# Optimization experiments

Hardware: AMD Instinct MI355X
Metric: run time of the kernel (lower is better)

Reference implementation:

```python
import jax, jax.numpy as jnp
import numpy as np

B, D = 65536, 1024
E, U, T = 10, 10, 2  # experts, expert units, tasks


def setup_inputs() -> dict:
    key = jax.random.key(0)
    ks = jax.random.split(key, 8)
    s = 0.02
    return {
        "x": jax.random.normal(ks[0], (B, D), dtype=jnp.float32),
        "show_index": jax.random.randint(ks[1], (B,), 0, 100),
        "st": jax.random.normal(ks[2], (B, 16), dtype=jnp.float32),
        "expert_w": jax.random.normal(ks[3], (E, D, U), dtype=jnp.float32) * s,
        "expert_b": jnp.zeros((E, U), dtype=jnp.float32),
        "gate_w": jax.random.normal(ks[4], (T, D, E), dtype=jnp.float32) * s,
        "gate_b": jnp.zeros((T, E), dtype=jnp.float32),
        "ctr_w": jax.random.normal(ks[5], (U, 1), dtype=jnp.float32) * s,
        "ctr_b": jnp.zeros((1,), dtype=jnp.float32),
        "cvr_w": jax.random.normal(ks[6], (U, 1), dtype=jnp.float32) * s,
        "cvr_b": jnp.zeros((1,), dtype=jnp.float32),
    }


def reference(x, show_index, st, expert_w, expert_b, gate_w, gate_b,
              ctr_w, ctr_b, cvr_w, cvr_b):
    # experts_output[b, u, e] = relu(x @ W_e + b_e)  (stacked on axis 2)
    experts_output = jax.nn.relu(
        jnp.einsum("bd,edu->bue", x, expert_w) + expert_b.T[None, :, :]
    )  # [B, U, E]
    # gates[b, t, e] = softmax over experts
    gates = jax.nn.softmax(
        jnp.einsum("bd,tde->bte", x, gate_w) + gate_b[None, :, :], axis=-1
    )  # [B, T, E]
    # weighted sum over experts for each task: [B, T, U]
    task_inputs = jnp.einsum("bue,bte->btu", experts_output, gates)
    ctr_logits = jax.nn.sigmoid(task_inputs[:, 0, :] @ ctr_w + ctr_b)  # [B, 1]
    cvr_logits = jax.nn.sigmoid(task_inputs[:, 1, :] @ cvr_w + cvr_b)  # [B, 1]
    return (ctr_logits, cvr_logits)
```

## Files before the change

kernel.cpp:

```cpp
#include <hip/hip_runtime.h>
#include <hip/hip_bf16.h>

#define B_ROWS 65536
#define D_DIM  1024
#define NC     120
#define NCP    128
#define MBLK   64
#define BK     64
#define ASTR   72
#define CSTR   121

typedef __attribute__((ext_vector_type(4))) float f32x4;
typedef __attribute__((ext_vector_type(8))) short bf16x8;

__device__ __forceinline__ unsigned short f2bf(float f) {
  union { float f; unsigned u; } v; v.f = f;
  unsigned r = v.u + 0x7FFFu + ((v.u >> 16) & 1u);
  return (unsigned short)(r >> 16);
}

__global__ __launch_bounds__(256) void pack_w(const float* __restrict__ ew,
                                              const float* __restrict__ gw,
                                              short* __restrict__ wt) {
  int idx = blockIdx.x * 256 + threadIdx.x;
  int c = idx >> 10, d = idx & 1023;
  float v = 0.f;
  if (c < 100) {
    int e = c / 10, u = c % 10;
    v = ew[(e * D_DIM + d) * 10 + u];
  } else if (c < NC) {
    int q = c - 100; int t = q / 10, e = q % 10;
    v = gw[(t * D_DIM + d) * 10 + e];
  }
  wt[c * D_DIM + d] = (short)f2bf(v);
}

union Smem {
  struct { short A[MBLK * ASTR]; short Bm[NCP * ASTR]; } s;
  float C[MBLK * CSTR];
};

__global__ __launch_bounds__(256) void mmoe_main(
    const float* __restrict__ x, const short* __restrict__ wt,
    const float* __restrict__ eb, const float* __restrict__ gb,
    const float* __restrict__ ctr_w, const float* __restrict__ ctr_b,
    const float* __restrict__ cvr_w, const float* __restrict__ cvr_b,
    float* __restrict__ out) {
  __shared__ Smem sm;
  const int tid  = threadIdx.x;
  const int wave = tid >> 6, lane = tid & 63;
  const int m0   = blockIdx.x * MBLK;

  const int arow = tid >> 4;
  const int akp  = (tid & 15) * 4;
  const int bc   = tid >> 3;
  const int bks  = (tid & 7) * 8;

  const int lhi = lane >> 4;
  const int llo = lane & 15;

  f32x4 acc[8];
  const f32x4 vzero = {0.f, 0.f, 0.f, 0.f};
  #pragma unroll
  for (int i = 0; i < 8; ++i) acc[i] = vzero;

  for (int k0 = 0; k0 < D_DIM; k0 += BK) {
    __syncthreads();
    #pragma unroll
    for (int j = 0; j < 4; ++j) {
      const int row = j * 16 + arow;
      const float4 v = *reinterpret_cast<const float4*>(
          x + (size_t)(m0 + row) * D_DIM + k0 + akp);
      ushort4 h;
      h.x = f2bf(v.x); h.y = f2bf(v.y); h.z = f2bf(v.z); h.w = f2bf(v.w);
      *reinterpret_cast<ushort4*>(&sm.s.A[row * ASTR + akp]) = h;
    }
    #pragma unroll
    for (int j = 0; j < 4; ++j) {
      const int c = j * 32 + bc;
      const uint4 v = *reinterpret_cast<const uint4*>(wt + c * D_DIM + k0 + bks);
      *reinterpret_cast<uint4*>(&sm.s.Bm[c * ASTR + bks]) = v;
    }
    __syncthreads();
    #pragma unroll
    for (int ks = 0; ks < BK; ks += 32) {
      const bf16x8 af = *reinterpret_cast<const bf16x8*>(
          &sm.s.A[(wave * 16 + llo) * ASTR + ks + lhi * 8]);
      #pragma unroll
      for (int ct = 0; ct < 8; ++ct) {
        const bf16x8 bf = *reinterpret_cast<const bf16x8*>(
            &sm.s.Bm[(ct * 16 + llo) * ASTR + ks + lhi * 8]);
        acc[ct] = __builtin_amdgcn_mfma_f32_16x16x32_bf16(af, bf, acc[ct], 0, 0, 0);
      }
    }
  }

  __syncthreads();
  #pragma unroll
  for (int ct = 0; ct < 8; ++ct) {
    const int col = ct * 16 + llo;
    if (col < NC) {
      #pragma unroll
      for (int r = 0; r < 4; ++r) {
        const int row = wave * 16 + lhi * 4 + r;
        sm.C[row * CSTR + col] = acc[ct][r];
      }
    }
  }
  __syncthreads();

  if (tid < MBLK) {
    const float* crow = &sm.C[tid * CSTR];
    float w0[10], w1[10];
    #pragma unroll
    for (int u = 0; u < 10; ++u) { w0[u] = ctr_w[u]; w1[u] = cvr_w[u]; }
    float s0[10], s1[10];
    #pragma unroll
    for (int e = 0; e < 10; ++e) {
      float a0 = 0.f, a1 = 0.f;
      #pragma unroll
      for (int u = 0; u < 10; ++u) {
        float v = crow[e * 10 + u] + eb[e * 10 + u];
        v = fmaxf(v, 0.f);
        a0 = fmaf(v, w0[u], a0);
        a1 = fmaf(v, w1[u], a1);
      }
      s0[e] = a0; s1[e] = a1;
    }
    {
      float gl[10], mx = -1e30f;
      #pragma unroll
      for (int e = 0; e < 10; ++e) { gl[e] = crow[100 + e] + gb[e]; mx = fmaxf(mx, gl[e]); }
      float den = 0.f, num = 0.f;
      #pragma unroll
      for (int e = 0; e < 10; ++e) {
        float p = __expf(gl[e] - mx); den += p; num = fmaf(p, s0[e], num);
      }
      float z = num / den + ctr_b[0];
      out[m0 + tid] = 1.f / (1.f + __expf(-z));
    }
    {
      float gl[10], mx = -1e30f;
      #pragma unroll
      for (int e = 0; e < 10; ++e) { gl[e] = crow[110 + e] + gb[10 + e]; mx = fmaxf(mx, gl[e]); }
      float den = 0.f, num = 0.f;
      #pragma unroll
      for (int e = 0; e < 10; ++e) {
        float p = __expf(gl[e] - mx); den += p; num = fmaf(p, s1[e], num);
      }
      float z = num / den + cvr_b[0];
      out[B_ROWS + m0 + tid] = 1.f / (1.f + __expf(-z));
    }
  }
}

extern "C" void kernel_launch(void* const* d_in, const int* in_sizes, int n_in,
                              void* d_out, int out_size, void* d_ws, size_t ws_size,
                              hipStream_t stream) {
  const float* x     = (const float*)d_in[0];
  const float* ew    = (const float*)d_in[3];
  const float* eb    = (const float*)d_in[4];
  const float* gw    = (const float*)d_in[5];
  const float* gb    = (const float*)d_in[6];
  const float* ctr_w = (const float*)d_in[7];
  const float* ctr_b = (const float*)d_in[8];
  const float* cvr_w = (const float*)d_in[9];
  const float* cvr_b = (const float*)d_in[10];
  float* out = (float*)d_out;
  short* wt  = (short*)d_ws;

  pack_w<<<512, 256, 0, stream>>>(ew, gw, wt);
  mmoe_main<<<B_ROWS / MBLK, 256, 0, stream>>>(x, wt, eb, gb, ctr_w, ctr_b,
                                               cvr_w, cvr_b, out);
}
```

Measured before the change: 398.1 us.

## Double-buffer weight tiles via direct global-to-LDS loads and register A operands

Replaces the single-buffered LDS staging of both x and weights with a two-stage pipeline. Weight tiles are copied straight into LDS with global_load_lds into an XOR-swizzled layout, prepared by the pack kernel, to avoid bank conflicts without padding. x is read directly into registers in MFMA operand order and converted to bf16 there, skipping the LDS round trip. The epilogue now splits the two tasks across 128 threads, and an occupancy hint of 4 blocks per CU is added, which costs more registers for the prefetched A fragments.

```diff
diff --git a/kernel.cpp b/kernel.cpp
--- a/kernel.cpp
+++ b/kernel.cpp
@@ -1,13 +1,10 @@
 #include <hip/hip_runtime.h>
-#include <hip/hip_bf16.h>
 
 #define B_ROWS 65536
 #define D_DIM  1024
 #define NC     120
-#define NCP    128
 #define MBLK   64
 #define BK     64
-#define ASTR   72
 #define CSTR   121
 
 typedef __attribute__((ext_vector_type(4))) float f32x4;
@@ -17,6 +14,15 @@
   union { float f; unsigned u; } v; v.f = f;
   unsigned r = v.u + 0x7FFFu + ((v.u >> 16) & 1u);
   return (unsigned short)(r >> 16);
+}
+
+__device__ __forceinline__ bf16x8 cvt8(float4 p, float4 q) {
+  bf16x8 r;
+  r[0] = (short)f2bf(p.x); r[1] = (short)f2bf(p.y);
+  r[2] = (short)f2bf(p.z); r[3] = (short)f2bf(p.w);
+  r[4] = (short)f2bf(q.x); r[5] = (short)f2bf(q.y);
+  r[6] = (short)f2bf(q.z); r[7] = (short)f2bf(q.w);
+  return r;
 }
 
 __global__ __launch_bounds__(256) void pack_w(const float* __restrict__ ew,
@@ -32,15 +38,22 @@
     int q = c - 100; int t = q / 10, e = q % 10;
     v = gw[(t * D_DIM + d) * 10 + e];
   }
-  wt[c * D_DIM + d] = (short)f2bf(v);
+  wt[c * D_DIM + (d ^ ((c & 7) << 3))] = (short)f2bf(v);
 }
 
-union Smem {
-  struct { short A[MBLK * ASTR]; short Bm[NCP * ASTR]; } s;
+union __align__(16) Smem {
+  struct { short B0[128 * 64]; short B1[128 * 64]; } s;
   float C[MBLK * CSTR];
 };
 
-__global__ __launch_bounds__(256) void mmoe_main(
+typedef const __attribute__((address_space(1))) void as1_cvoid;
+typedef __attribute__((address_space(3))) void as3_void;
+
+__device__ __forceinline__ void gload_lds16(const void* g, void* l) {
+  __builtin_amdgcn_global_load_lds((as1_cvoid*)g, (as3_void*)l, 16, 0, 0);
+}
+
+__global__ __launch_bounds__(256, 4) void mmoe_main(
     const float* __restrict__ x, const short* __restrict__ wt,
     const float* __restrict__ eb, const float* __restrict__ gb,
     const float* __restrict__ ctr_w, const float* __restrict__ ctr_b,
@@ -49,108 +62,115 @@
   __shared__ Smem sm;
   const int tid  = threadIdx.x;
   const int wave = tid >> 6, lane = tid & 63;
+  const int lhi  = lane >> 4, llo = lane & 15;
   const int m0   = blockIdx.x * MBLK;
+  const int bswz = (llo & 7) << 3;
 
-  const int arow = tid >> 4;
-  const int akp  = (tid & 15) * 4;
-  const int bc   = tid >> 3;
-  const int bks  = (tid & 7) * 8;
+  const float* ax = x + (size_t)(m0 + wave * 16 + llo) * D_DIM + lhi * 8;
 
-  const int lhi = lane >> 4;
-  const int llo = lane & 15;
+  const short* bsrc = wt + (lane >> 3) * D_DIM + (lane & 7) * 8;
+  short* const b0p = sm.s.B0 + wave * 2048 + lane * 8;
+  short* const b1p = sm.s.B1 + wave * 2048 + lane * 8;
 
   f32x4 acc[8];
-  const f32x4 vzero = {0.f, 0.f, 0.f, 0.f};
   #pragma unroll
-  for (int i = 0; i < 8; ++i) acc[i] = vzero;
+  for (int i = 0; i < 8; ++i) acc[i] = (f32x4){0.f, 0.f, 0.f, 0.f};
+  float4 a0[4], a1[4];
 
-  for (int k0 = 0; k0 < D_DIM; k0 += BK) {
+#define STAGE0(K0) do { _Pragma("unroll") \
+    for (int j = 0; j < 4; ++j) \
+      gload_lds16(bsrc + (wave * 4 + j) * 8 * D_DIM + (K0), b0p + j * 512); \
+  } while (0)
+#define STAGE1(K0) do { _Pragma("unroll") \
+    for (int j = 0; j < 4; ++j) \
+      gload_lds16(bsrc + (wave * 4 + j) * 8 * D_DIM + (K0), b1p + j * 512); \
+  } while (0)
+#define LOADA(AR, K0) do { \
+    AR[0] = *reinterpret_cast<const float4*>(ax + (K0)); \
+    AR[1] = *reinterpret_cast<const float4*>(ax + (K0) + 4); \
+    AR[2] = *reinterpret_cast<const float4*>(ax + (K0) + 32); \
+    AR[3] = *reinterpret_cast<const float4*>(ax + (K0) + 36); \
+  } while (0)
+#define COMPUTE(BUF, AR) do { \
+    const bf16x8 af0 = cvt8(AR[0], AR[1]); \
+    const bf16x8 af1 = cvt8(AR[2], AR[3]); \
+    _Pragma("unroll") \
+    for (int ct = 0; ct < 8; ++ct) { \
+      const bf16x8 b = *reinterpret_cast<const bf16x8*>( \
+          (BUF) + (ct * 16 + llo) * 64 + ((lhi * 8) ^ bswz)); \
+      acc[ct] = __builtin_amdgcn_mfma_f32_16x16x32_bf16(af0, b, acc[ct], 0, 0, 0); \
+    } \
+    _Pragma("unroll") \
+    for (int ct = 0; ct < 8; ++ct) { \
+      const bf16x8 b = *reinterpret_cast<const bf16x8*>( \
+          (BUF) + (ct * 16 + llo) * 64 + ((32 + lhi * 8) ^ bswz)); \
+      acc[ct] = __builtin_amdgcn_mfma_f32_16x16x32_bf16(af1, b, acc[ct], 0, 0, 0); \
+    } \
+  } while (0)
+
+  STAGE0(0);
+  LOADA(a0, 0);
+  __syncthreads();
+
+  #pragma unroll
+  for (int tt = 0; tt < 8; ++tt) {
+    const int t = 2 * tt;
+    LOADA(a1, (t + 1) * BK);
+    STAGE1((t + 1) * BK);
+    COMPUTE(sm.s.B0, a0);
     __syncthreads();
-    #pragma unroll
-    for (int j = 0; j < 4; ++j) {
-      const int row = j * 16 + arow;
-      const float4 v = *reinterpret_cast<const float4*>(
-          x + (size_t)(m0 + row) * D_DIM + k0 + akp);
-      ushort4 h;
-      h.x = f2bf(v.x); h.y = f2bf(v.y); h.z = f2bf(v.z); h.w = f2bf(v.w);
-      *reinterpret_cast<ushort4*>(&sm.s.A[row * ASTR + akp]) = h;
+    if (tt < 7) {
+      LOADA(a0, (t + 2) * BK);
+      STAGE0((t + 2) * BK);
     }
-    #pragma unroll
-    for (int j = 0; j < 4; ++j) {
-      const int c = j * 32 + bc;
-      const uint4 v = *reinterpret_cast<const uint4*>(wt + c * D_DIM + k0 + bks);
-      *reinterpret_cast<uint4*>(&sm.s.Bm[c * ASTR + bks]) = v;
-    }
+    COMPUTE(sm.s.B1, a1);
     __syncthreads();
-    #pragma unroll
-    for (int ks = 0; ks < BK; ks += 32) {
-      const bf16x8 af = *reinterpret_cast<const bf16x8*>(
-          &sm.s.A[(wave * 16 + llo) * ASTR + ks + lhi * 8]);
-      #pragma unroll
-      for (int ct = 0; ct < 8; ++ct) {
-        const bf16x8 bf = *reinterpret_cast<const bf16x8*>(
-            &sm.s.Bm[(ct * 16 + llo) * ASTR + ks + lhi * 8]);
-        acc[ct] = __builtin_amdgcn_mfma_f32_16x16x32_bf16(af, bf, acc[ct], 0, 0, 0);
-      }
-    }
   }
 
-  __syncthreads();
   #pragma unroll
   for (int ct = 0; ct < 8; ++ct) {
     const int col = ct * 16 + llo;
     if (col < NC) {
       #pragma unroll
-      for (int r = 0; r < 4; ++r) {
-        const int row = wave * 16 + lhi * 4 + r;
-        sm.C[row * CSTR + col] = acc[ct][r];
-      }
+      for (int r = 0; r < 4; ++r)
+        sm.C[(wave * 16 + lhi * 4 + r) * CSTR + col] = acc[ct][r];
     }
   }
   __syncthreads();
 
-  if (tid < MBLK) {
-    const float* crow = &sm.C[tid * CSTR];
-    float w0[10], w1[10];
+  if (tid < 2 * MBLK) {
+    const int task = tid >> 6, row = tid & 63;
+    const float* crow = &sm.C[row * CSTR];
+    const float* wv = task ? cvr_w : ctr_w;
+    const float  bv = task ? cvr_b[0] : ctr_b[0];
+    float w[10];
     #pragma unroll
-    for (int u = 0; u < 10; ++u) { w0[u] = ctr_w[u]; w1[u] = cvr_w[u]; }
-    float s0[10], s1[10];
+    for (int u = 0; u < 10; ++u) w[u] = wv[u];
+    float s[10];
     #pragma unroll
     for (int e = 0; e < 10; ++e) {
-      float a0 = 0.f, a1 = 0.f;
+      float a = 0.f;
       #pragma unroll
       for (int u = 0; u < 10; ++u) {
-        float v = crow[e * 10 + u] + eb[e * 10 + u];
-        v = fmaxf(v, 0.f);
-        a0 = fmaf(v, w0[u], a0);
-        a1 = fmaf(v, w1[u], a1);
+        float v = fmaxf(crow[e * 10 + u] + eb[e * 10 + u], 0.f);
+        a = fmaf(v, w[u], a);
       }
-      s0[e] = a0; s1[e] = a1;
+      s[e] = a;
     }
-    {
-      float gl[10], mx = -1e30f;
-      #pragma unroll
-      for (int e = 0; e < 10; ++e) { gl[e] = crow[100 + e] + gb[e]; mx = fmaxf(mx, gl[e]); }
-      float den = 0.f, num = 0.f;
-      #pragma unroll
-      for (int e = 0; e < 10; ++e) {
-        float p = __expf(gl[e] - mx); den += p; num = fmaf(p, s0[e], num);
-      }
-      float z = num / den + ctr_b[0];
-      out[m0 + tid] = 1.f / (1.f + __expf(-z));
+    float gl[10], mx = -1e30f;
+    #pragma unroll
+    for (int e = 0; e < 10; ++e) {
+      gl[e] = crow[100 + task * 10 + e] + gb[task * 10 + e];
+      mx = fmaxf(mx, gl[e]);
     }
-    {
-      float gl[10], mx = -1e30f;
-      #pragma unroll
-      for (int e = 0; e < 10; ++e) { gl[e] = crow[110 + e] + gb[10 + e]; mx = fmaxf(mx, gl[e]); }
-      float den = 0.f, num = 0.f;
-      #pragma unroll
-      for (int e = 0; e < 10; ++e) {
-        float p = __expf(gl[e] - mx); den += p; num = fmaf(p, s1[e], num);
-      }
-      float z = num / den + cvr_b[0];
-      out[B_ROWS + m0 + tid] = 1.f / (1.f + __expf(-z));
+    float den = 0.f, num = 0.f;
+    #pragma unroll
+    for (int e = 0; e < 10; ++e) {
+      float p = __expf(gl[e] - mx);
+      den += p; num = fmaf(p, s[e], num);
     }
+    float z = num / den + bv;
+    out[task * B_ROWS + m0 + row] = 1.f / (1.f + __expf(-z));
   }
 }
 
```

Result: no change. 396.4 us (-0.4%).
